# Optimization experiments

Measured on AMD Instinct MI355X. Metric: run time of the kernel, lower is better.

The kernel has to match this reference:

```python
import jax, jax.numpy as jnp
import numpy as np

D_MODEL = 512
D_QK = 512
H = 8
HEAD_DIM = D_QK // H   # 64
V_DIM = D_MODEL // H   # 64
PROJ_OUT = D_MODEL + 2 * D_QK + H  # 1544


def setup_inputs() -> dict:
    key = jax.random.key(0)
    k1, k2, k3, k4, k5 = jax.random.split(key, 5)
    B, S = 2, 2048
    x = jax.random.normal(k1, (B, S, D_MODEL), dtype=jnp.float32)
    s_in = 1.0 / np.sqrt(D_MODEL)
    Wvqkn_w = jax.random.uniform(k2, (PROJ_OUT, D_MODEL), jnp.float32, -s_in, s_in)
    Wvqkn_b = jax.random.uniform(k3, (PROJ_OUT,), jnp.float32, -s_in, s_in)
    out_w = jax.random.uniform(k4, (D_MODEL, D_MODEL), jnp.float32, -s_in, s_in)
    out_b = jax.random.uniform(k5, (D_MODEL,), jnp.float32, -s_in, s_in)
    return {"x": x, "Wvqkn_w": Wvqkn_w, "Wvqkn_b": Wvqkn_b,
            "out_w": out_w, "out_b": out_b}


def reference(x, Wvqkn_w, Wvqkn_b, out_w, out_b):
    B, S, _ = x.shape
    # fused qkvn projection
    vqkn = jnp.einsum('bsd,od->bso', x, Wvqkn_w) + Wvqkn_b  # [B,S,1544]
    v = vqkn[..., :D_MODEL]                                  # [B,S,512]
    qk = vqkn[..., D_MODEL:D_MODEL + 2 * D_QK]               # [B,S,1024]
    n = vqkn[..., D_MODEL + 2 * D_QK:]                       # [B,S,H]
    qk = qk.reshape(B, S, 2, H, HEAD_DIM)
    v = v.reshape(B, S, H, V_DIM)
    q, k = qk[:, :, 0], qk[:, :, 1]                          # approx_fn = identity
    # linear attention via cumulative KV state (scale=1.0, scale_B=False)
    kv = jnp.einsum('bshd,bsht->bshdt', k, v)                # [B,S,H,D,Dv]
    kv = jnp.cumsum(kv, axis=1)
    out = jnp.einsum('bshd,bshdt->bsht', q, kv)              # [B,S,H,Dv]
    # normalization gating: norm_fn = exp, no offset
    gate = jnp.exp(-jnp.exp(n))                              # [B,S,H]
    ctx = gate[..., None] * out
    ctx = ctx.reshape(B, S, D_MODEL)
    return jnp.einsum('bsd,od->bso', ctx, out_w) + out_b
```

## Files before the change

### kernel.cpp

```cpp
#include <hip/hip_runtime.h>
#include <hip/hip_bf16.h>
#include <math.h>

#define B_    2
#define S_    2048
#define DM    512
#define H_    8
#define PROJ  1544
#define NPAD1 1664
#define CHK   64
#define NC    32
#define BS_   4096
#define BH    16

typedef __attribute__((ext_vector_type(8))) short shortx8;
typedef __attribute__((ext_vector_type(4))) short shortx4;
typedef __attribute__((ext_vector_type(4))) float floatx4;

#define GCAST(p) ((const __attribute__((address_space(1))) void*)(p))
#define LCAST(p) ((__attribute__((address_space(3))) void*)(p))

__device__ inline short f2bf(float f) {
    __hip_bfloat16 h = __float2bfloat16(f);
    return *(short*)&h;
}
__device__ inline float bf2f(short s) {
    __hip_bfloat16 h = *(__hip_bfloat16*)&s;
    return __bfloat162float(h);
}
__device__ inline shortx8 read8(const short* buf, int row, int k) {
    return *(const shortx8*)&buf[row * 64 + ((((k >> 3) ^ (row & 7))) << 3)];
}

#define E1 ((size_t)BS_ * DM)
#define E2 ((size_t)NPAD1 * DM)
#define E3 ((size_t)DM * DM)
__global__ __launch_bounds__(256) void convert_all(const float* __restrict__ x,
                                                   const float* __restrict__ w1,
                                                   const float* __restrict__ w2,
                                                   short* __restrict__ xb,
                                                   short* __restrict__ w1b,
                                                   short* __restrict__ w2b) {
    size_t e = ((size_t)blockIdx.x * 256 + threadIdx.x) * 8;
    const float* src;
    short* dst;
    bool zero = false;
    if (e < E1) { src = x + e; dst = xb + e; }
    else if (e < E1 + E2) {
        size_t o = e - E1;
        dst = w1b + o;
        size_t row = o >> 9;
        if (row < PROJ) src = w1 + o; else { src = w1; zero = true; }
    } else if (e < E1 + E2 + E3) {
        size_t o = e - E1 - E2;
        src = w2 + o; dst = w2b + o;
    } else return;
    short out[8];
    if (zero) {
#pragma unroll
        for (int i = 0; i < 8; i++) out[i] = 0;
    } else {
        float4 f0 = *(const float4*)src;
        float4 f1 = *(const float4*)(src + 4);
        out[0] = f2bf(f0.x); out[1] = f2bf(f0.y); out[2] = f2bf(f0.z); out[3] = f2bf(f0.w);
        out[4] = f2bf(f1.x); out[5] = f2bf(f1.y); out[6] = f2bf(f1.z); out[7] = f2bf(f1.w);
    }
    *(shortx8*)dst = *(shortx8*)out;
}

__global__ __launch_bounds__(256) void gemm_mfma64(const short* __restrict__ A,
                                                   const short* __restrict__ Bw,
                                                   const float* __restrict__ bias,
                                                   float* __restrict__ C,
                                                   int N, int K) {
    __shared__ __align__(16) short As[64 * 64];
    __shared__ __align__(16) short Bs[128 * 64];
    const int tid  = threadIdx.x;
    const int wave = tid >> 6, lane = tid & 63;
    const int m0 = blockIdx.y * 64;
    const int n0 = blockIdx.x * 128;
    const int lrow = lane >> 3;
    const int swz  = ((lane & 7) ^ lrow) << 3;
    const int lm = lane & 15, q = lane >> 4;
    const int wc = wave * 32;
    floatx4 acc[4][2] = {};

    const short* gA0 = A  + (size_t)(m0 +      wave * 8 + lrow) * K + swz;
    const short* gA1 = A  + (size_t)(m0 + 32 + wave * 8 + lrow) * K + swz;
    const short* gB[4];
#pragma unroll
    for (int h = 0; h < 4; h++)
        gB[h] = Bw + (size_t)(n0 + h * 32 + wave * 8 + lrow) * K + swz;

    for (int k0 = 0; k0 < K; k0 += 64) {
        __builtin_amdgcn_global_load_lds(GCAST(gA0 + k0), LCAST(&As[(wave * 8) * 64]),        16, 0, 0);
        __builtin_amdgcn_global_load_lds(GCAST(gA1 + k0), LCAST(&As[(32 + wave * 8) * 64]),   16, 0, 0);
#pragma unroll
        for (int h = 0; h < 4; h++)
            __builtin_amdgcn_global_load_lds(GCAST(gB[h] + k0), LCAST(&Bs[(h * 32 + wave * 8) * 64]), 16, 0, 0);
        __syncthreads();
        shortx8 af[2][4], bw[2][2];
#pragma unroll
        for (int ks = 0; ks < 2; ks++) {
#pragma unroll
            for (int i = 0; i < 4; i++) af[ks][i] = read8(As, i * 16 + lm, ks * 32 + q * 8);
#pragma unroll
            for (int j = 0; j < 2; j++) bw[ks][j] = read8(Bs, wc + j * 16 + lm, ks * 32 + q * 8);
        }
#pragma unroll
        for (int ks = 0; ks < 2; ks++)
#pragma unroll
            for (int i = 0; i < 4; i++)
#pragma unroll
                for (int j = 0; j < 2; j++)
                    acc[i][j] = __builtin_amdgcn_mfma_f32_16x16x32_bf16(af[ks][i], bw[ks][j], acc[i][j], 0, 0, 0);
        __syncthreads();
    }
#pragma unroll
    for (int i = 0; i < 4; i++) {
        int rb = m0 + i * 16 + q * 4;
#pragma unroll
        for (int j = 0; j < 2; j++) {
            int col = n0 + wc + j * 16 + lm;
            float bv = bias[col];
#pragma unroll
            for (int r = 0; r < 4; r++)
                C[(size_t)(rb + r) * N + col] = acc[i][j][r] + bv;
        }
    }
}

__global__ __launch_bounds__(256) void gemm1_fused(const short* __restrict__ A,
                                                   const short* __restrict__ Bw,
                                                   const float* __restrict__ bias,
                                                   short* __restrict__ qb,
                                                   short* __restrict__ kb,
                                                   short* __restrict__ kTb,
                                                   short* __restrict__ vTb,
                                                   float* __restrict__ gateb) {
    __shared__ __align__(16) short As[128 * 64];
    __shared__ __align__(16) short Bs[128 * 64];
    const int K = DM;
    const int tid  = threadIdx.x;
    const int wave = tid >> 6, lane = tid & 63;
    const int m0 = blockIdx.y * 128;
    const int n0 = blockIdx.x * 128;
    const int lrow = lane >> 3;
    const int swz  = ((lane & 7) ^ lrow) << 3;
    const int lm = lane & 15, q = lane >> 4;
    const int wr = (wave >> 1) * 64;
    const int wc = (wave & 1) * 64;
    floatx4 acc[4][4] = {};

    const short* gA[4];
    const short* gB[4];
#pragma unroll
    for (int g = 0; g < 4; g++)
        gA[g] = A  + (size_t)(m0 + g * 32 + wave * 8 + lrow) * K + swz;
#pragma unroll
    for (int h = 0; h < 4; h++)
        gB[h] = Bw + (size_t)(n0 + h * 32 + wave * 8 + lrow) * K + swz;

    for (int k0 = 0; k0 < K; k0 += 64) {
#pragma unroll
        for (int g = 0; g < 4; g++)
            __builtin_amdgcn_global_load_lds(GCAST(gA[g] + k0), LCAST(&As[(g * 32 + wave * 8) * 64]), 16, 0, 0);
#pragma unroll
        for (int h = 0; h < 4; h++)
            __builtin_amdgcn_global_load_lds(GCAST(gB[h] + k0), LCAST(&Bs[(h * 32 + wave * 8) * 64]), 16, 0, 0);
        __syncthreads();
        shortx8 af[2][4], bw[2][4];
#pragma unroll
        for (int ks = 0; ks < 2; ks++) {
#pragma unroll
            for (int i = 0; i < 4; i++) af[ks][i] = read8(As, wr + i * 16 + lm, ks * 32 + q * 8);
#pragma unroll
            for (int j = 0; j < 4; j++) bw[ks][j] = read8(Bs, wc + j * 16 + lm, ks * 32 + q * 8);
        }
#pragma unroll
        for (int ks = 0; ks < 2; ks++)
#pragma unroll
            for (int i = 0; i < 4; i++)
#pragma unroll
                for (int j = 0; j < 4; j++)
                    acc[i][j] = __builtin_amdgcn_mfma_f32_16x16x32_bf16(af[ks][i], bw[ks][j], acc[i][j], 0, 0, 0);
        __syncthreads();
    }

    const int bIdx = m0 >> 11;
    const int bh0  = bIdx * H_;
#pragma unroll
    for (int i = 0; i < 4; i++) {
        int s0 = (m0 & (S_ - 1)) + wr + i * 16 + q * 4;
#pragma unroll
        for (int j = 0; j < 4; j++) {
            int col = n0 + wc + j * 16 + lm;
            float bv = (col < PROJ) ? bias[col] : 0.f;
            float vals[4];
#pragma unroll
            for (int r = 0; r < 4; r++) vals[r] = acc[i][j][r] + bv;
            if (col < 512) {
                int h = col >> 6, vd = col & 63;
                short tmp[4];
#pragma unroll
                for (int r = 0; r < 4; r++) tmp[r] = f2bf(vals[r]);
                *(shortx4*)&vTb[((size_t)(bh0 + h) * 64 + vd) * S_ + s0] = *(shortx4*)tmp;
            } else if (col < 1024) {
                int h = (col >> 6) - 8, d = col & 63;
                size_t rb = ((size_t)(bh0 + h) * S_ + s0) * 64 + d;
#pragma unroll
                for (int r = 0; r < 4; r++) qb[rb + (size_t)r * 64] = f2bf(vals[r]);
            } else if (col < 1536) {
                int h = (col >> 6) - 16, d = col & 63;
                size_t rb = ((size_t)(bh0 + h) * S_ + s0) * 64 + d;
                short tmp[4];
#pragma unroll
                for (int r = 0; r < 4; r++) { tmp[r] = f2bf(vals[r]); kb[rb + (size_t)r * 64] = tmp[r]; }
                *(shortx4*)&kTb[((size_t)(bh0 + h) * 64 + d) * S_ + s0] = *(shortx4*)tmp;
            } else if (col < PROJ) {
                int h = col - 1536;
                float g[4];
#pragma unroll
                for (int r = 0; r < 4; r++) g[r] = __expf(-__expf(vals[r]));
                *(float4*)&gateb[(size_t)(bh0 + h) * S_ + s0] = make_float4(g[0], g[1], g[2], g[3]);
            }
        }
    }
}

__global__ __launch_bounds__(256) void chunk_kv_mfma(const short* __restrict__ vTb,
                                                     const short* __restrict__ kTb,
                                                     float* __restrict__ kvbuf) {
    __shared__ __align__(16) short VT[64 * 64];
    __shared__ __align__(16) short KT[64 * 64];
    const int blk = blockIdx.x;
    const int c = blk & (NC - 1), bh = blk >> 5;
    const int base = c * CHK;
    const int tid = threadIdx.x, wave = tid >> 6, lane = tid & 63;
    const int lrow = lane >> 3, lgrp = lane & 7;

#pragma unroll
    for (int half = 0; half < 2; half++) {
        int v0 = wave * 8 + half * 32;
        int row = v0 + lrow;
        int gcol = ((lgrp ^ (row & 7)) << 3);
        __builtin_amdgcn_global_load_lds(GCAST(vTb + ((size_t)(bh * 64 + row)) * S_ + base + gcol),
                                         LCAST(&VT[v0 * 64]), 16, 0, 0);
        __builtin_amdgcn_global_load_lds(GCAST(kTb + ((size_t)(bh * 64 + row)) * S_ + base + gcol),
                                         LCAST(&KT[v0 * 64]), 16, 0, 0);
    }
    __syncthreads();

    const int lm = lane & 15, q = lane >> 4;
    const int wr = (wave >> 1) * 32, wc = (wave & 1) * 32;
    floatx4 acc[2][2] = {};
#pragma unroll
    for (int ks = 0; ks < 2; ks++) {
        shortx8 a[2], b2[2];
#pragma unroll
        for (int i = 0; i < 2; i++) a[i]  = read8(VT, wr + i * 16 + lm, ks * 32 + q * 8);
#pragma unroll
        for (int j = 0; j < 2; j++) b2[j] = read8(KT, wc + j * 16 + lm, ks * 32 + q * 8);
#pragma unroll
        for (int i = 0; i < 2; i++)
#pragma unroll
            for (int j = 0; j < 2; j++)
                acc[i][j] = __builtin_amdgcn_mfma_f32_16x16x32_bf16(a[i], b2[j], acc[i][j], 0, 0, 0);
    }
    float* outp = kvbuf + ((size_t)blk << 12);
#pragma unroll
    for (int i = 0; i < 2; i++)
#pragma unroll
        for (int j = 0; j < 2; j++)
#pragma unroll
            for (int r = 0; r < 4; r++)
                outp[(wr + i * 16 + q * 4 + r) * 64 + wc + j * 16 + lm] = acc[i][j][r];
}

__global__ __launch_bounds__(256) void scan_groups(const float* __restrict__ kvbuf,
                                                   float* __restrict__ kvg) {
    const int blk = blockIdx.x;
    const int bh = blk >> 4, seg = blk & 15;
    const int e = seg * 256 + threadIdx.x;
    const float* src = kvbuf + (((size_t)bh * NC) << 12) + e;
    float* dst = kvg + (((size_t)bh * 8) << 12) + e;
    float run = 0.f;
#pragma unroll
    for (int g = 0; g < 8; g++) {
        dst[(size_t)g << 12] = run;
#pragma unroll
        for (int cc = 0; cc < 4; cc++)
            run += src[(size_t)(g * 4 + cc) << 12];
    }
}

__global__ __launch_bounds__(256) void attn_mfma(const short* __restrict__ qb,
                                                 const short* __restrict__ kb,
                                                 const short* __restrict__ vTb,
                                                 const float* __restrict__ gateb,
                                                 const float* __restrict__ kvbuf,
                                                 const float* __restrict__ kvg,
                                                 short* __restrict__ ctxb) {
    __shared__ __align__(16) short Qs[64 * 64];
    __shared__ __align__(16) short Ks[64 * 64];
    __shared__ __align__(16) short VTs[64 * 64];
    __shared__ __align__(16) short Phi[64 * 64];
    __shared__ __align__(16) short Plo[64 * 64];
    __shared__ __align__(16) short Sb[64 * 72];
    __shared__ float gs[64];
    const int blk = blockIdx.x;
    const int bh = blk & (BH - 1);
    const int c  = (NC - 1) - (blk >> 4);
    const int base = c * CHK;
    const int tid = threadIdx.x, wave = tid >> 6, lane = tid & 63;
    const int lrow = lane >> 3, lgrp = lane & 7;

#pragma unroll
    for (int half = 0; half < 2; half++) {
        int v0 = wave * 8 + half * 32;
        int row = v0 + lrow;
        int gcol = ((lgrp ^ (row & 7)) << 3);
        __builtin_amdgcn_global_load_lds(GCAST(qb + ((size_t)bh * S_ + base + row) * 64 + gcol),
                                         LCAST(&Qs[v0 * 64]), 16, 0, 0);
        __builtin_amdgcn_global_load_lds(GCAST(kb + ((size_t)bh * S_ + base + row) * 64 + gcol),
                                         LCAST(&Ks[v0 * 64]), 16, 0, 0);
        __builtin_amdgcn_global_load_lds(GCAST(vTb + ((size_t)(bh * 64 + row)) * S_ + base + gcol),
                                         LCAST(&VTs[v0 * 64]), 16, 0, 0);
    }

    float pacc[16];
    {
        const float* gp = kvg + (((size_t)bh * 8 + (c >> 2)) << 12) + tid;
#pragma unroll
        for (int it = 0; it < 16; it++) pacc[it] = gp[it * 256];
        const float* kvb = kvbuf + (((size_t)bh * NC) << 12) + tid;
        for (int cp = c & ~3; cp < c; cp++) {
            const float* p = kvb + ((size_t)cp << 12);
#pragma unroll
            for (int it = 0; it < 16; it++) pacc[it] += p[it * 256];
        }
    }
#pragma unroll
    for (int it = 0; it < 16; it++) {
        int idx = it * 256 + tid;
        int v = idx >> 6, d = idx & 63;
        float f = pacc[it];
        short hi = f2bf(f);
        short lo = f2bf(f - bf2f(hi));
        int sw = v * 64 + (((d >> 3) ^ (v & 7)) << 3) + (d & 7);
        Phi[sw] = hi; Plo[sw] = lo;
    }
    if (tid < 64) gs[tid] = gateb[(size_t)bh * S_ + base + tid];
    __syncthreads();

    const int lm = lane & 15, q = lane >> 4;
    const int wr = (wave >> 1) * 32, wc = (wave & 1) * 32;

    floatx4 sacc[2][2] = {};
#pragma unroll
    for (int ks = 0; ks < 2; ks++) {
        shortx8 qa[2], kf[2];
#pragma unroll
        for (int i = 0; i < 2; i++) qa[i] = read8(Qs, wr + i * 16 + lm, ks * 32 + q * 8);
#pragma unroll
        for (int j = 0; j < 2; j++) kf[j] = read8(Ks, wc + j * 16 + lm, ks * 32 + q * 8);
#pragma unroll
        for (int i = 0; i < 2; i++)
#pragma unroll
            for (int j = 0; j < 2; j++)
                sacc[i][j] = __builtin_amdgcn_mfma_f32_16x16x32_bf16(qa[i], kf[j], sacc[i][j], 0, 0, 0);
    }
#pragma unroll
    for (int i = 0; i < 2; i++)
#pragma unroll
        for (int j = 0; j < 2; j++)
#pragma unroll
            for (int r = 0; r < 4; r++) {
                int s = wr + i * 16 + q * 4 + r;
                int t = wc + j * 16 + lm;
                Sb[s * 72 + t] = f2bf(t <= s ? sacc[i][j][r] : 0.f);
            }
    __syncthreads();

    floatx4 oacc[2][2] = {};
#pragma unroll
    for (int ks = 0; ks < 2; ks++) {
        shortx8 sa[2], vb[2];
#pragma unroll
        for (int i = 0; i < 2; i++)
            sa[i] = *(const shortx8*)&Sb[(wr + i * 16 + lm) * 72 + ks * 32 + q * 8];
#pragma unroll
        for (int j = 0; j < 2; j++) vb[j] = read8(VTs, wc + j * 16 + lm, ks * 32 + q * 8);
#pragma unroll
        for (int i = 0; i < 2; i++)
#pragma unroll
            for (int j = 0; j < 2; j++)
                oacc[i][j] = __builtin_amdgcn_mfma_f32_16x16x32_bf16(sa[i], vb[j], oacc[i][j], 0, 0, 0);
    }
#pragma unroll
    for (int ks = 0; ks < 2; ks++) {
        shortx8 qa[2], ph[2], pl[2];
#pragma unroll
        for (int i = 0; i < 2; i++) qa[i] = read8(Qs, wr + i * 16 + lm, ks * 32 + q * 8);
#pragma unroll
        for (int j = 0; j < 2; j++) {
            ph[j] = read8(Phi, wc + j * 16 + lm, ks * 32 + q * 8);
            pl[j] = read8(Plo, wc + j * 16 + lm, ks * 32 + q * 8);
        }
#pragma unroll
        for (int i = 0; i < 2; i++)
#pragma unroll
            for (int j = 0; j < 2; j++) {
                oacc[i][j] = __builtin_amdgcn_mfma_f32_16x16x32_bf16(qa[i], ph[j], oacc[i][j], 0, 0, 0);
                oacc[i][j] = __builtin_amdgcn_mfma_f32_16x16x32_bf16(qa[i], pl[j], oacc[i][j], 0, 0, 0);
            }
    }
    const size_t tok0 = (size_t)(bh >> 3) * S_ + base;
    const int h = bh & 7;
#pragma unroll
    for (int i = 0; i < 2; i++)
#pragma unroll
        for (int j = 0; j < 2; j++)
#pragma unroll
            for (int r = 0; r < 4; r++) {
                int s = wr + i * 16 + q * 4 + r;
                int v = wc + j * 16 + lm;
                ctxb[(tok0 + s) * DM + h * 64 + v] = f2bf(gs[s] * oacc[i][j][r]);
            }
}

extern "C" void kernel_launch(void* const* d_in, const int* in_sizes, int n_in,
                              void* d_out, int out_size, void* d_ws, size_t ws_size,
                              hipStream_t stream) {
    const float* x       = (const float*)d_in[0];
    const float* Wvqkn_w = (const float*)d_in[1];
    const float* Wvqkn_b = (const float*)d_in[2];
    const float* out_w   = (const float*)d_in[3];
    const float* out_b   = (const float*)d_in[4];
    float* out = (float*)d_out;

    float* kvbuf = (float*)d_ws;
    float* kvg   = kvbuf + (size_t)BH * NC * 4096;
    short* xb    = (short*)(kvg + (size_t)BH * 8 * 4096);
    short* w1b   = xb   + (size_t)BS_ * DM;
    short* w2b   = w1b  + (size_t)NPAD1 * DM;
    short* ctxb  = w2b  + (size_t)DM * DM;
    short* qb    = ctxb + (size_t)BS_ * DM;
    short* kb    = qb   + (size_t)BH * S_ * 64;
    short* kTb   = kb   + (size_t)BH * S_ * 64;
    short* vTb   = kTb  + (size_t)BH * S_ * 64;
    float* gateb = (float*)(vTb + (size_t)BH * S_ * 64);

    convert_all<<<(int)((E1 + E2 + E3) / 8 / 256), 256, 0, stream>>>(
        x, Wvqkn_w, out_w, xb, w1b, w2b);

    gemm1_fused<<<dim3(NPAD1 / 128, BS_ / 128), 256, 0, stream>>>(
        xb, w1b, Wvqkn_b, qb, kb, kTb, vTb, gateb);

    chunk_kv_mfma<<<BH * NC, 256, 0, stream>>>(vTb, kTb, kvbuf);
    scan_groups<<<BH * 16, 256, 0, stream>>>(kvbuf, kvg);
    attn_mfma<<<BH * NC, 256, 0, stream>>>(qb, kb, vTb, gateb, kvbuf, kvg, ctxb);

    gemm_mfma64<<<dim3(DM / 128, BS_ / 64), 256, 0, stream>>>(ctxb, w2b, out_b, out, DM, DM);
}
```

Measured before the change: 112.7 us.

## Fuse all six kernels into one cooperative persistent kernel with grid syncs

Measured after the change: 418.5 us. +271.5%, slower.

```diff
diff --git a/kernel.cpp b/kernel.cpp
--- a/kernel.cpp
+++ b/kernel.cpp
@@ -1,6 +1,9 @@
 #include <hip/hip_runtime.h>
 #include <hip/hip_bf16.h>
+#include <hip/hip_cooperative_groups.h>
 #include <math.h>
+
+namespace cg = cooperative_groups;
 
 #define B_    2
 #define S_    2048
@@ -35,6 +38,375 @@
 #define E1 ((size_t)BS_ * DM)
 #define E2 ((size_t)NPAD1 * DM)
 #define E3 ((size_t)DM * DM)
+
+__global__ __launch_bounds__(256, 2) void mega(
+        const float* __restrict__ x,  const float* __restrict__ w1,
+        const float* __restrict__ w2, const float* __restrict__ bias1,
+        const float* __restrict__ bias2,
+        short* __restrict__ xb, short* __restrict__ w1b, short* __restrict__ w2b,
+        short* __restrict__ qb, short* __restrict__ kb, short* __restrict__ kTb,
+        short* __restrict__ vTb, float* __restrict__ gateb,
+        float* __restrict__ kvbuf, float* __restrict__ kvg,
+        short* __restrict__ ctxb, float* __restrict__ out) {
+    __shared__ __align__(16) char smem[50432];
+    cg::grid_group grid = cg::this_grid();
+    const int blk  = blockIdx.x;
+    const int tid  = threadIdx.x;
+    const int wave = tid >> 6, lane = tid & 63;
+    const int lrow = lane >> 3, lgrp = lane & 7;
+    const int lm = lane & 15, q = lane >> 4;
+
+    for (size_t c = (size_t)blk * 256 + tid; c < (E1 + E2 + E3) / 8; c += 512 * 256) {
+        size_t e = c * 8;
+        const float* src;
+        short* dst;
+        bool zero = false;
+        if (e < E1) { src = x + e; dst = xb + e; }
+        else if (e < E1 + E2) {
+            size_t o = e - E1;
+            dst = w1b + o;
+            size_t row = o >> 9;
+            if (row < PROJ) src = w1 + o; else { src = w1; zero = true; }
+        } else {
+            size_t o = e - E1 - E2;
+            src = w2 + o; dst = w2b + o;
+        }
+        short o8[8];
+        if (zero) {
+#pragma unroll
+            for (int i = 0; i < 8; i++) o8[i] = 0;
+        } else {
+            float4 f0 = *(const float4*)src;
+            float4 f1 = *(const float4*)(src + 4);
+            o8[0] = f2bf(f0.x); o8[1] = f2bf(f0.y); o8[2] = f2bf(f0.z); o8[3] = f2bf(f0.w);
+            o8[4] = f2bf(f1.x); o8[5] = f2bf(f1.y); o8[6] = f2bf(f1.z); o8[7] = f2bf(f1.w);
+        }
+        *(shortx8*)dst = *(shortx8*)o8;
+    }
+    grid.sync();
+
+    if (blk < 416) {
+        short* As = (short*)smem;
+        short* Bs = (short*)(smem + 16384);
+        const int K  = DM;
+        const int bx = blk % 13, by = blk / 13;
+        const int m0 = by * 128, n0 = bx * 128;
+        const int swz = ((lane & 7) ^ lrow) << 3;
+        const int wr = (wave >> 1) * 64, wc = (wave & 1) * 64;
+        floatx4 acc[4][4] = {};
+
+        const short* gA[4];
+        const short* gB[4];
+#pragma unroll
+        for (int g = 0; g < 4; g++)
+            gA[g] = xb + (size_t)(m0 + g * 32 + wave * 8 + lrow) * K + swz;
+#pragma unroll
+        for (int h = 0; h < 4; h++)
+            gB[h] = w1b + (size_t)(n0 + h * 32 + wave * 8 + lrow) * K + swz;
+
+        for (int k0 = 0; k0 < K; k0 += 64) {
+#pragma unroll
+            for (int g = 0; g < 4; g++)
+                __builtin_amdgcn_global_load_lds(GCAST(gA[g] + k0), LCAST(&As[(g * 32 + wave * 8) * 64]), 16, 0, 0);
+#pragma unroll
+            for (int h = 0; h < 4; h++)
+                __builtin_amdgcn_global_load_lds(GCAST(gB[h] + k0), LCAST(&Bs[(h * 32 + wave * 8) * 64]), 16, 0, 0);
+            __syncthreads();
+            shortx8 af[2][4], bw[2][4];
+#pragma unroll
+            for (int ks = 0; ks < 2; ks++) {
+#pragma unroll
+                for (int i = 0; i < 4; i++) af[ks][i] = read8(As, wr + i * 16 + lm, ks * 32 + q * 8);
+#pragma unroll
+                for (int j = 0; j < 4; j++) bw[ks][j] = read8(Bs, wc + j * 16 + lm, ks * 32 + q * 8);
+            }
+#pragma unroll
+            for (int ks = 0; ks < 2; ks++)
+#pragma unroll
+                for (int i = 0; i < 4; i++)
+#pragma unroll
+                    for (int j = 0; j < 4; j++)
+                        acc[i][j] = __builtin_amdgcn_mfma_f32_16x16x32_bf16(af[ks][i], bw[ks][j], acc[i][j], 0, 0, 0);
+            __syncthreads();
+        }
+
+        const int bIdx = m0 >> 11;
+        const int bh0  = bIdx * H_;
+#pragma unroll
+        for (int i = 0; i < 4; i++) {
+            int s0 = (m0 & (S_ - 1)) + wr + i * 16 + q * 4;
+#pragma unroll
+            for (int j = 0; j < 4; j++) {
+                int col = n0 + wc + j * 16 + lm;
+                float bv = (col < PROJ) ? bias1[col] : 0.f;
+                float vals[4];
+#pragma unroll
+                for (int r = 0; r < 4; r++) vals[r] = acc[i][j][r] + bv;
+                if (col < 512) {
+                    int h = col >> 6, vd = col & 63;
+                    short tmp[4];
+#pragma unroll
+                    for (int r = 0; r < 4; r++) tmp[r] = f2bf(vals[r]);
+                    *(shortx4*)&vTb[((size_t)(bh0 + h) * 64 + vd) * S_ + s0] = *(shortx4*)tmp;
+                } else if (col < 1024) {
+                    int h = (col >> 6) - 8, d = col & 63;
+                    size_t rb = ((size_t)(bh0 + h) * S_ + s0) * 64 + d;
+#pragma unroll
+                    for (int r = 0; r < 4; r++) qb[rb + (size_t)r * 64] = f2bf(vals[r]);
+                } else if (col < 1536) {
+                    int h = (col >> 6) - 16, d = col & 63;
+                    size_t rb = ((size_t)(bh0 + h) * S_ + s0) * 64 + d;
+                    short tmp[4];
+#pragma unroll
+                    for (int r = 0; r < 4; r++) { tmp[r] = f2bf(vals[r]); kb[rb + (size_t)r * 64] = tmp[r]; }
+                    *(shortx4*)&kTb[((size_t)(bh0 + h) * 64 + d) * S_ + s0] = *(shortx4*)tmp;
+                } else if (col < PROJ) {
+                    int h = col - 1536;
+                    float g[4];
+#pragma unroll
+                    for (int r = 0; r < 4; r++) g[r] = __expf(-__expf(vals[r]));
+                    *(float4*)&gateb[(size_t)(bh0 + h) * S_ + s0] = make_float4(g[0], g[1], g[2], g[3]);
+                }
+            }
+        }
+    }
+    grid.sync();
+
+    {
+        short* VT = (short*)smem;
+        short* KT = (short*)(smem + 8192);
+        const int c = blk & (NC - 1), bh = blk >> 5;
+        const int base = c * CHK;
+#pragma unroll
+        for (int half = 0; half < 2; half++) {
+            int v0 = wave * 8 + half * 32;
+            int row = v0 + lrow;
+            int gcol = ((lgrp ^ (row & 7)) << 3);
+            __builtin_amdgcn_global_load_lds(GCAST(vTb + ((size_t)(bh * 64 + row)) * S_ + base + gcol),
+                                             LCAST(&VT[v0 * 64]), 16, 0, 0);
+            __builtin_amdgcn_global_load_lds(GCAST(kTb + ((size_t)(bh * 64 + row)) * S_ + base + gcol),
+                                             LCAST(&KT[v0 * 64]), 16, 0, 0);
+        }
+        __syncthreads();
+        const int wr = (wave >> 1) * 32, wc = (wave & 1) * 32;
+        floatx4 acc[2][2] = {};
+#pragma unroll
+        for (int ks = 0; ks < 2; ks++) {
+            shortx8 a[2], b2[2];
+#pragma unroll
+            for (int i = 0; i < 2; i++) a[i]  = read8(VT, wr + i * 16 + lm, ks * 32 + q * 8);
+#pragma unroll
+            for (int j = 0; j < 2; j++) b2[j] = read8(KT, wc + j * 16 + lm, ks * 32 + q * 8);
+#pragma unroll
+            for (int i = 0; i < 2; i++)
+#pragma unroll
+                for (int j = 0; j < 2; j++)
+                    acc[i][j] = __builtin_amdgcn_mfma_f32_16x16x32_bf16(a[i], b2[j], acc[i][j], 0, 0, 0);
+        }
+        float* outp = kvbuf + ((size_t)blk << 12);
+#pragma unroll
+        for (int i = 0; i < 2; i++)
+#pragma unroll
+            for (int j = 0; j < 2; j++)
+#pragma unroll
+                for (int r = 0; r < 4; r++)
+                    outp[(wr + i * 16 + q * 4 + r) * 64 + wc + j * 16 + lm] = acc[i][j][r];
+    }
+    grid.sync();
+
+    if (blk < 256) {
+        const int bh = blk >> 4, seg = blk & 15;
+        const int e = seg * 256 + tid;
+        const float* src = kvbuf + (((size_t)bh * NC) << 12) + e;
+        float* dst = kvg + (((size_t)bh * 8) << 12) + e;
+        float run = 0.f;
+#pragma unroll
+        for (int g = 0; g < 8; g++) {
+            dst[(size_t)g << 12] = run;
+#pragma unroll
+            for (int cc = 0; cc < 4; cc++)
+                run += src[(size_t)(g * 4 + cc) << 12];
+        }
+    }
+    grid.sync();
+
+    {
+        short* Qs  = (short*)smem;
+        short* Ks  = (short*)(smem + 8192);
+        short* VTs = (short*)(smem + 16384);
+        short* Phi = (short*)(smem + 24576);
+        short* Plo = (short*)(smem + 32768);
+        short* Sb  = (short*)(smem + 40960);
+        float* gs  = (float*)(smem + 50176);
+        const int bh = blk & (BH - 1);
+        const int c  = (NC - 1) - (blk >> 4);
+        const int base = c * CHK;
+
+#pragma unroll
+        for (int half = 0; half < 2; half++) {
+            int v0 = wave * 8 + half * 32;
+            int row = v0 + lrow;
+            int gcol = ((lgrp ^ (row & 7)) << 3);
+            __builtin_amdgcn_global_load_lds(GCAST(qb + ((size_t)bh * S_ + base + row) * 64 + gcol),
+                                             LCAST(&Qs[v0 * 64]), 16, 0, 0);
+            __builtin_amdgcn_global_load_lds(GCAST(kb + ((size_t)bh * S_ + base + row) * 64 + gcol),
+                                             LCAST(&Ks[v0 * 64]), 16, 0, 0);
+            __builtin_amdgcn_global_load_lds(GCAST(vTb + ((size_t)(bh * 64 + row)) * S_ + base + gcol),
+                                             LCAST(&VTs[v0 * 64]), 16, 0, 0);
+        }
+
+        float pacc[16];
+        {
+            const float* gp = kvg + (((size_t)bh * 8 + (c >> 2)) << 12) + tid;
+#pragma unroll
+            for (int it = 0; it < 16; it++) pacc[it] = gp[it * 256];
+            const float* kvb = kvbuf + (((size_t)bh * NC) << 12) + tid;
+            for (int cp = c & ~3; cp < c; cp++) {
+                const float* p = kvb + ((size_t)cp << 12);
+#pragma unroll
+                for (int it = 0; it < 16; it++) pacc[it] += p[it * 256];
+            }
+        }
+#pragma unroll
+        for (int it = 0; it < 16; it++) {
+            int idx = it * 256 + tid;
+            int v = idx >> 6, d = idx & 63;
+            float f = pacc[it];
+            short hi = f2bf(f);
+            short lo = f2bf(f - bf2f(hi));
+            int sw = v * 64 + (((d >> 3) ^ (v & 7)) << 3) + (d & 7);
+            Phi[sw] = hi; Plo[sw] = lo;
+        }
+        if (tid < 64) gs[tid] = gateb[(size_t)bh * S_ + base + tid];
+        __syncthreads();
+
+        const int wr = (wave >> 1) * 32, wc = (wave & 1) * 32;
+
+        floatx4 sacc[2][2] = {};
+#pragma unroll
+        for (int ks = 0; ks < 2; ks++) {
+            shortx8 qa[2], kf[2];
+#pragma unroll
+            for (int i = 0; i < 2; i++) qa[i] = read8(Qs, wr + i * 16 + lm, ks * 32 + q * 8);
+#pragma unroll
+            for (int j = 0; j < 2; j++) kf[j] = read8(Ks, wc + j * 16 + lm, ks * 32 + q * 8);
+#pragma unroll
+            for (int i = 0; i < 2; i++)
+#pragma unroll
+                for (int j = 0; j < 2; j++)
+                    sacc[i][j] = __builtin_amdgcn_mfma_f32_16x16x32_bf16(qa[i], kf[j], sacc[i][j], 0, 0, 0);
+        }
+#pragma unroll
+        for (int i = 0; i < 2; i++)
+#pragma unroll
+            for (int j = 0; j < 2; j++)
+#pragma unroll
+                for (int r = 0; r < 4; r++) {
+                    int s = wr + i * 16 + q * 4 + r;
+                    int t = wc + j * 16 + lm;
+                    Sb[s * 72 + t] = f2bf(t <= s ? sacc[i][j][r] : 0.f);
+                }
+        __syncthreads();
+
+        floatx4 oacc[2][2] = {};
+#pragma unroll
+        for (int ks = 0; ks < 2; ks++) {
+            shortx8 sa[2], vb[2];
+#pragma unroll
+            for (int i = 0; i < 2; i++)
+                sa[i] = *(const shortx8*)&Sb[(wr + i * 16 + lm) * 72 + ks * 32 + q * 8];
+#pragma unroll
+            for (int j = 0; j < 2; j++) vb[j] = read8(VTs, wc + j * 16 + lm, ks * 32 + q * 8);
+#pragma unroll
+            for (int i = 0; i < 2; i++)
+#pragma unroll
+                for (int j = 0; j < 2; j++)
+                    oacc[i][j] = __builtin_amdgcn_mfma_f32_16x16x32_bf16(sa[i], vb[j], oacc[i][j], 0, 0, 0);
+        }
+#pragma unroll
+        for (int ks = 0; ks < 2; ks++) {
+            shortx8 qa[2], ph[2], pl[2];
+#pragma unroll
+            for (int i = 0; i < 2; i++) qa[i] = read8(Qs, wr + i * 16 + lm, ks * 32 + q * 8);
+#pragma unroll
+            for (int j = 0; j < 2; j++) {
+                ph[j] = read8(Phi, wc + j * 16 + lm, ks * 32 + q * 8);
+                pl[j] = read8(Plo, wc + j * 16 + lm, ks * 32 + q * 8);
+            }
+#pragma unroll
+            for (int i = 0; i < 2; i++)
+#pragma unroll
+                for (int j = 0; j < 2; j++) {
+                    oacc[i][j] = __builtin_amdgcn_mfma_f32_16x16x32_bf16(qa[i], ph[j], oacc[i][j], 0, 0, 0);
+                    oacc[i][j] = __builtin_amdgcn_mfma_f32_16x16x32_bf16(qa[i], pl[j], oacc[i][j], 0, 0, 0);
+                }
+        }
+        const size_t tok0 = (size_t)(bh >> 3) * S_ + base;
+        const int h = bh & 7;
+#pragma unroll
+        for (int i = 0; i < 2; i++)
+#pragma unroll
+            for (int j = 0; j < 2; j++)
+#pragma unroll
+                for (int r = 0; r < 4; r++) {
+                    int s = wr + i * 16 + q * 4 + r;
+                    int v = wc + j * 16 + lm;
+                    ctxb[(tok0 + s) * DM + h * 64 + v] = f2bf(gs[s] * oacc[i][j][r]);
+                }
+    }
+    grid.sync();
+
+    {
+        short* As = (short*)smem;
+        short* Bs = (short*)(smem + 8192);
+        const int m0 = (blk >> 3) * 64;
+        const int n0 = (blk & 7) * 64;
+        const int swz = (lgrp ^ lrow) << 3;
+        const int wr = (wave >> 1) * 32, wc = (wave & 1) * 32;
+        floatx4 acc[2][2] = {};
+        for (int k0 = 0; k0 < DM; k0 += 64) {
+#pragma unroll
+            for (int half = 0; half < 2; half++) {
+                int r0 = wave * 8 + half * 32;
+                int row = r0 + lrow;
+                __builtin_amdgcn_global_load_lds(GCAST(ctxb + (size_t)(m0 + row) * DM + k0 + swz),
+                                                 LCAST(&As[r0 * 64]), 16, 0, 0);
+                __builtin_amdgcn_global_load_lds(GCAST(w2b + (size_t)(n0 + row) * DM + k0 + swz),
+                                                 LCAST(&Bs[r0 * 64]), 16, 0, 0);
+            }
+            __syncthreads();
+            shortx8 a2[2][2], b2[2][2];
+#pragma unroll
+            for (int ks = 0; ks < 2; ks++) {
+#pragma unroll
+                for (int i = 0; i < 2; i++) a2[ks][i] = read8(As, wr + i * 16 + lm, ks * 32 + q * 8);
+#pragma unroll
+                for (int j = 0; j < 2; j++) b2[ks][j] = read8(Bs, wc + j * 16 + lm, ks * 32 + q * 8);
+            }
+#pragma unroll
+            for (int ks = 0; ks < 2; ks++)
+#pragma unroll
+                for (int i = 0; i < 2; i++)
+#pragma unroll
+                    for (int j = 0; j < 2; j++)
+                        acc[i][j] = __builtin_amdgcn_mfma_f32_16x16x32_bf16(a2[ks][i], b2[ks][j], acc[i][j], 0, 0, 0);
+            __syncthreads();
+        }
+#pragma unroll
+        for (int i = 0; i < 2; i++) {
+            int rb = m0 + wr + i * 16 + q * 4;
+#pragma unroll
+            for (int j = 0; j < 2; j++) {
+                int col = n0 + wc + j * 16 + lm;
+                float bv = bias2[col];
+#pragma unroll
+                for (int r = 0; r < 4; r++)
+                    out[(size_t)(rb + r) * DM + col] = acc[i][j][r] + bv;
+            }
+        }
+    }
+}
+
 __global__ __launch_bounds__(256) void convert_all(const float* __restrict__ x,
                                                    const float* __restrict__ w1,
                                                    const float* __restrict__ w2,
@@ -451,15 +823,22 @@
     short* vTb   = kTb  + (size_t)BH * S_ * 64;
     float* gateb = (float*)(vTb + (size_t)BH * S_ * 64);
 
-    convert_all<<<(int)((E1 + E2 + E3) / 8 / 256), 256, 0, stream>>>(
-        x, Wvqkn_w, out_w, xb, w1b, w2b);
-
-    gemm1_fused<<<dim3(NPAD1 / 128, BS_ / 128), 256, 0, stream>>>(
-        xb, w1b, Wvqkn_b, qb, kb, kTb, vTb, gateb);
-
-    chunk_kv_mfma<<<BH * NC, 256, 0, stream>>>(vTb, kTb, kvbuf);
-    scan_groups<<<BH * 16, 256, 0, stream>>>(kvbuf, kvg);
-    attn_mfma<<<BH * NC, 256, 0, stream>>>(qb, kb, vTb, gateb, kvbuf, kvg, ctxb);
-
-    gemm_mfma64<<<dim3(DM / 128, BS_ / 64), 256, 0, stream>>>(ctxb, w2b, out_b, out, DM, DM);
-}
+    void* args[] = {
+        (void*)&x, (void*)&Wvqkn_w, (void*)&out_w, (void*)&Wvqkn_b, (void*)&out_b,
+        (void*)&xb, (void*)&w1b, (void*)&w2b,
+        (void*)&qb, (void*)&kb, (void*)&kTb, (void*)&vTb, (void*)&gateb,
+        (void*)&kvbuf, (void*)&kvg, (void*)&ctxb, (void*)&out
+    };
+    hipError_t err = hipLaunchCooperativeKernel((const void*)mega, dim3(512), dim3(256),
+                                                args, 0, stream);
+    if (err != hipSuccess) {
+        convert_all<<<(int)((E1 + E2 + E3) / 8 / 256), 256, 0, stream>>>(
+            x, Wvqkn_w, out_w, xb, w1b, w2b);
+        gemm1_fused<<<dim3(NPAD1 / 128, BS_ / 128), 256, 0, stream>>>(
+            xb, w1b, Wvqkn_b, qb, kb, kTb, vTb, gateb);
+        chunk_kv_mfma<<<BH * NC, 256, 0, stream>>>(vTb, kTb, kvbuf);
+        scan_groups<<<BH * 16, 256, 0, stream>>>(kvbuf, kvg);
+        attn_mfma<<<BH * NC, 256, 0, stream>>>(qb, kb, vTb, gateb, kvbuf, kvg, ctxb);
+        gemm_mfma64<<<dim3(DM / 128, BS_ / 64), 256, 0, stream>>>(ctxb, w2b, out_b, out, DM, DM);
+    }
+}
```
